# Kernel optimization log

Measured on AMD Instinct MI355X. Metric: run time of the kernel, lower is better.

The kernel has to match this reference:

```python
import jax, jax.numpy as jnp
import numpy as np

B, G, T, C = 32, 4, 512, 256


def setup_inputs() -> dict:
    key = jax.random.key(0)
    k1, k2, k3 = jax.random.split(key, 3)
    x = jax.random.normal(k1, (B, G, T, C), dtype=jnp.float32)
    # learned per-channel params, initialized around the repo defaults 0.3 / 0.1
    w_input = 0.3 * jax.random.uniform(k2, (C,), dtype=jnp.float32) + 0.15
    w_leak = 0.1 * jax.random.uniform(k3, (C,), dtype=jnp.float32) + 0.05
    return {"x": x, "w_input": w_input, "w_leak": w_leak}


def _heaviside(v):
    # theta_forget: step function with zero gradient (matches @tf.custom_gradient)
    return jax.lax.stop_gradient((v >= 0).astype(v.dtype))


def reference(x, w_input, w_leak):
    # x: (B, G, T, C) -> flatten group into batch, scan over time
    b, g, t, c = x.shape
    V_THRESH = 1.0   # V_thresh default
    T_REF = 1.0      # t_refrectory receives self.thresh (=1) positionally
    xr = jnp.transpose(x.reshape(b * g, t, c), (1, 0, 2))  # (T, N, C)

    def step(carry, xt):
        Vm, R = carry
        R = _heaviside(Vm - V_THRESH) * T_REF + _heaviside(R - 1.0) * (R - 1.0)
        Vm = (w_input * xt + (1.0 - w_leak) * Vm) * _heaviside(-R)
        return (Vm, R), Vm

    zeros = jnp.zeros((b * g, c), dtype=x.dtype)
    _, Vs = jax.lax.scan(step, (zeros, zeros), xr)  # Vs: (T, N, C)
    return jnp.transpose(Vs, (1, 0, 2)).reshape(b, g, t, c)
```

## Files before the change

kernel.cpp:

```cpp
#include <hip/hip_runtime.h>


constexpr int T_STEPS = 512;
constexpr int CCH     = 256;
constexpr int NSEQ    = 128;
constexpr int WIN     = 16;
constexpr int K       = 4;
constexpr int NW      = T_STEPS / WIN;

__device__ __forceinline__ void sfence() { __builtin_amdgcn_sched_barrier(0); }

__global__ __launch_bounds__(320, 1) void lif_kernel(
    const float* __restrict__ x,
    const float* __restrict__ w_input,
    const float* __restrict__ w_leak,
    float* __restrict__ out)
{
#pragma clang fp contract(off)
    __shared__ float xw[K][WIN * CCH];

    const int tid  = threadIdx.x;
    const int wv   = tid >> 6;
    const int lane = tid & 63;
    const int n    = blockIdx.x;

    if (wv == 4) {
        const float* xg = x + (size_t)n * T_STEPS * CCH + lane * 4;
        auto issue = [&](int W) {
            const float* s0 = xg + (size_t)W * WIN * CCH;
            float* d0 = &xw[W & 3][0];
#pragma unroll
            for (int i = 0; i < WIN; ++i) {
                __builtin_amdgcn_global_load_lds(
                    (const __attribute__((address_space(1))) void*)(s0 + i * CCH),
                    (__attribute__((address_space(3))) void*)(d0 + i * CCH),
                    16, 0, 0);
            }
            sfence();
        };

        issue(0); issue(1); issue(2);
        for (int W = 0; W < NW; ++W) {
            const int rem = NW - 1 - W;
            if (rem >= 2)      asm volatile("s_waitcnt vmcnt(32)" ::: "memory");
            else if (rem == 1) asm volatile("s_waitcnt vmcnt(16)" ::: "memory");
            else               asm volatile("s_waitcnt vmcnt(0)"  ::: "memory");
            sfence();
            __builtin_amdgcn_s_barrier();
            sfence();
            if (W + 3 < NW) issue(W + 3);
        }
    } else {
        const int ch = wv * 64 + lane;
        const float w = w_input[ch];
        const float a = 1.0f - w_leak[ch];
        float* og = out + (size_t)n * T_STEPS * CCH + ch;
        float Vm = 0.0f;

        for (int W = 0; W < NW; ++W) {
            sfence();
            __builtin_amdgcn_s_barrier();
            sfence();
            const float* xb = &xw[W & 3][0];
#pragma unroll
            for (int k = 0; k < WIN; ++k) {
                const float xt = xb[k * CCH + ch];
                const float v = (w * xt) + (a * Vm);
                Vm = (Vm - 1.0f >= 0.0f) ? 0.0f : v;
                og[(size_t)(W * WIN + k) * CCH] = Vm;
            }
            sfence();
        }
    }
}

extern "C" void kernel_launch(void* const* d_in, const int* in_sizes, int n_in,
                              void* d_out, int out_size, void* d_ws, size_t ws_size,
                              hipStream_t stream) {
    const float* x       = (const float*)d_in[0];
    const float* w_input = (const float*)d_in[1];
    const float* w_leak  = (const float*)d_in[2];
    float* out = (float*)d_out;

    dim3 grid(NSEQ);
    dim3 block(320);
    hipLaunchKernelGGL(lif_kernel, grid, block, 0, stream,
                       x, w_input, w_leak, out);
}
```

Before: 26.09 us.

## Split channels across two blocks per sequence and deepen LDS prefetch ring

The grid doubles from 128 to 256 blocks, and each block now covers half the channels (128) of one sequence, so more CUs hold work. The block shrinks to two compute waves plus one loader wave. The shared-memory ring grows from 4 to 8 windows with 6 windows in flight, and the vmcnt waits are adjusted to match. Each loader lane now fetches half-rows, so the row-stride and LDS addressing change, with more per-block issue overhead in exchange for more parallel sequential scans.

```diff
diff --git a/kernel.cpp b/kernel.cpp
--- a/kernel.cpp
+++ b/kernel.cpp
@@ -3,55 +3,64 @@
 
 constexpr int T_STEPS = 512;
 constexpr int CCH     = 256;
-constexpr int NSEQ    = 128;
+constexpr int HCH     = 128;
 constexpr int WIN     = 16;
-constexpr int K       = 4;
+constexpr int K       = 8;
 constexpr int NW      = T_STEPS / WIN;
 
 __device__ __forceinline__ void sfence() { __builtin_amdgcn_sched_barrier(0); }
 
-__global__ __launch_bounds__(320, 1) void lif_kernel(
+__global__ __launch_bounds__(192, 1) void lif_kernel(
     const float* __restrict__ x,
     const float* __restrict__ w_input,
     const float* __restrict__ w_leak,
     float* __restrict__ out)
 {
 #pragma clang fp contract(off)
-    __shared__ float xw[K][WIN * CCH];
+    __shared__ float xw[K][WIN * HCH];
 
     const int tid  = threadIdx.x;
     const int wv   = tid >> 6;
     const int lane = tid & 63;
-    const int n    = blockIdx.x;
+    const int b    = blockIdx.x;
+    const int n    = b & 127;
+    const int h    = b >> 7;
 
-    if (wv == 4) {
-        const float* xg = x + (size_t)n * T_STEPS * CCH + lane * 4;
+    const float* xg0 = x + (size_t)n * T_STEPS * CCH + h * HCH;
+
+    if (wv == 2) {
+        const float* xl = xg0 + (lane >> 5) * CCH + (lane & 31) * 4;
         auto issue = [&](int W) {
-            const float* s0 = xg + (size_t)W * WIN * CCH;
-            float* d0 = &xw[W & 3][0];
+            const float* s0 = xl + (size_t)W * WIN * CCH;
+            float* d0 = &xw[W & 7][0];
 #pragma unroll
-            for (int i = 0; i < WIN; ++i) {
+            for (int i = 0; i < 8; ++i) {
                 __builtin_amdgcn_global_load_lds(
-                    (const __attribute__((address_space(1))) void*)(s0 + i * CCH),
-                    (__attribute__((address_space(3))) void*)(d0 + i * CCH),
+                    (const __attribute__((address_space(1))) void*)(s0 + (size_t)(2 * i) * CCH),
+                    (__attribute__((address_space(3))) void*)(d0 + i * 256),
                     16, 0, 0);
             }
             sfence();
         };
 
-        issue(0); issue(1); issue(2);
+        issue(0); issue(1); issue(2); issue(3); issue(4); issue(5);
         for (int W = 0; W < NW; ++W) {
             const int rem = NW - 1 - W;
-            if (rem >= 2)      asm volatile("s_waitcnt vmcnt(32)" ::: "memory");
-            else if (rem == 1) asm volatile("s_waitcnt vmcnt(16)" ::: "memory");
-            else               asm volatile("s_waitcnt vmcnt(0)"  ::: "memory");
+            const int o = rem < 5 ? rem : 5;
+            if      (o == 5) asm volatile("s_waitcnt vmcnt(40)" ::: "memory");
+            else if (o == 4) asm volatile("s_waitcnt vmcnt(32)" ::: "memory");
+            else if (o == 3) asm volatile("s_waitcnt vmcnt(24)" ::: "memory");
+            else if (o == 2) asm volatile("s_waitcnt vmcnt(16)" ::: "memory");
+            else if (o == 1) asm volatile("s_waitcnt vmcnt(8)"  ::: "memory");
+            else             asm volatile("s_waitcnt vmcnt(0)"  ::: "memory");
             sfence();
             __builtin_amdgcn_s_barrier();
             sfence();
-            if (W + 3 < NW) issue(W + 3);
+            if (W + 6 < NW) issue(W + 6);
         }
     } else {
-        const int ch = wv * 64 + lane;
+        const int cidx = wv * 64 + lane;
+        const int ch   = h * HCH + cidx;
         const float w = w_input[ch];
         const float a = 1.0f - w_leak[ch];
         float* og = out + (size_t)n * T_STEPS * CCH + ch;
@@ -61,10 +70,10 @@
             sfence();
             __builtin_amdgcn_s_barrier();
             sfence();
-            const float* xb = &xw[W & 3][0];
+            const float* xb = &xw[W & 7][0];
 #pragma unroll
             for (int k = 0; k < WIN; ++k) {
-                const float xt = xb[k * CCH + ch];
+                const float xt = xb[k * HCH + cidx];
                 const float v = (w * xt) + (a * Vm);
                 Vm = (Vm - 1.0f >= 0.0f) ? 0.0f : v;
                 og[(size_t)(W * WIN + k) * CCH] = Vm;
@@ -82,8 +91,8 @@
     const float* w_leak  = (const float*)d_in[2];
     float* out = (float*)d_out;
 
-    dim3 grid(NSEQ);
-    dim3 block(320);
+    dim3 grid(256);
+    dim3 block(192);
     hipLaunchKernelGGL(lif_kernel, grid, block, 0, stream,
                        x, w_input, w_leak, out);
 }
```

Result: slower. 26.82 us (+2.8%).
